# Performance work log

Measured on AMD Instinct MI355X. Metric: run time of the kernel, lower is better.

Reference implementation:

```python
import jax, jax.numpy as jnp
import numpy as np

B = 1024
P = 8
D = 2048
NUM_IDS = 64
MARGIN = 0.3
EPS = 1e-12


def setup_inputs() -> dict:
    key = jax.random.key(0)
    k1, k2, k3 = jax.random.split(key, 3)
    feats = jax.random.normal(k1, (B, P * D), dtype=jnp.float32)
    labels = jax.random.randint(k2, (B,), 0, NUM_IDS, dtype=jnp.int64)
    subs = jax.random.randint(k3, (B,), 0, 2, dtype=jnp.int64)
    return {"feats": feats, "labels": labels, "subs": subs}


def reference(feats, labels, subs):
    b = feats.shape[0]
    f = feats.reshape(b, -1, D)  # [B, P, D]
    dt = f.dtype

    # Per-sample class centers via a single segment-mean pass
    # (equivalent to the original per-sample boolean-mask mean loop).
    seg_sum = jax.ops.segment_sum(f, labels, num_segments=NUM_IDS)  # [NUM_IDS, P, D]
    counts = jax.ops.segment_sum(jnp.ones((b,), dt), labels, num_segments=NUM_IDS)
    centers_by_id = seg_sum / jnp.maximum(counts, 1.0)[:, None, None]
    centers = centers_by_id[labels]  # [B, P, D]

    # dist_ap[i] = sum_p ||f[i,p] - center[i,p]||
    d_ap = jnp.sqrt(jnp.clip(jnp.sum((f - centers) ** 2, axis=-1), EPS, None)).sum(-1)  # [B]
    dist_ap = d_ap[:, None] + d_ap[None, :]  # [B, B]

    # pairwise_distance: dist_aa[i,j] = sum_p ||f[i,p] - f[j,p]||, via gemm trick
    sq = jnp.sum(f * f, axis=-1)  # [B, P]
    inner = jnp.einsum('ipd,jpd->ijp', f, f)  # [B, B, P]
    d2 = sq[:, None, :] + sq[None, :, :] - 2.0 * inner
    dist_aa = jnp.sqrt(jnp.clip(d2, EPS, None)).sum(-1)  # [B, B]

    # masked margin loss over negative (different-label) pairs
    mask = labels[:, None] != labels[None, :]  # [B, B] bool
    vals = jnp.clip(dist_ap - dist_aa + MARGIN, 0.0, None)
    maskf = mask.astype(dt)
    loss = jnp.sum(vals * maskf) / jnp.sum(maskf)
    return loss
```

## Files before the change

### kernel.cpp

```cpp
#include <hip/hip_runtime.h>
#include <hip/hip_bf16.h>

#define B_ 1024
#define P_ 8
#define D_ 2048
#define FD_ (P_ * D_)
#define NID 64
#define MARGIN_ 0.3f
#define EPS_ 1e-12f

typedef unsigned short u16;
typedef float float4_t __attribute__((ext_vector_type(4)));

#define AS1 __attribute__((address_space(1)))
#define AS3 __attribute__((address_space(3)))

__device__ __forceinline__ float bf2f(u16 v) {
    unsigned x = (unsigned)v << 16;
    float f;
    __builtin_memcpy(&f, &x, 4);
    return f;
}

static const size_t OFF_COUNTS = 0;
static const size_t OFF_OFFS   = 256;
static const size_t OFF_PERM   = 512;
static const size_t OFF_NEG    = 4608;
static const size_t OFF_POS    = 8176;
static const size_t OFF_S      = 8192;
static const size_t OFF_SQ     = 40960;
static const size_t OFF_DAP    = 73728;
static const size_t OFF_FB     = 131072;
static const size_t OFF_PD     = OFF_FB + (size_t)B_ * FD_;

__global__ void k_counts(const int* __restrict__ labels, float* countsf, int* offs,
                         int* perm, float* negcnt) {
    __shared__ int h[NID], o[NID], cur[NID];
    int tid = threadIdx.x;
    if (tid < NID) h[tid] = 0;
    __syncthreads();
    for (int i = tid; i < B_; i += 256) atomicAdd(&h[labels[i]], 1);
    __syncthreads();
    if (tid == 0) {
        int acc = 0;
        long long ss = 0;
        for (int c = 0; c < NID; c++) {
            o[c] = acc;
            acc += h[c];
            ss += (long long)h[c] * h[c];
        }
        *negcnt = (float)((long long)B_ * B_ - ss);
    }
    __syncthreads();
    if (tid < NID) {
        countsf[tid] = (float)h[tid];
        offs[tid] = o[tid];
        cur[tid] = o[tid];
    }
    __syncthreads();
    for (int i = tid; i < B_; i += 256) {
        int pos = atomicAdd(&cur[labels[i]], 1);
        perm[pos] = i;
    }
}

__global__ void k_rowstats(const float* __restrict__ feats, unsigned char* __restrict__ fb,
                           float* __restrict__ sq) {
    int i = blockIdx.x;
    int tid = threadIdx.x;
    int w = tid >> 6, lane = tid & 63;
    const float* frow = feats + (size_t)i * FD_;
    unsigned char* brow = fb + (size_t)i * FD_;
#pragma unroll
    for (int pp = 0; pp < 2; pp++) {
        int p = w * 2 + pp;
        int off = p * D_;
        float s2 = 0.f;
#pragma unroll
        for (int ch = 0; ch < 8; ch++) {
            int d = off + ch * 256 + lane * 4;
            float4 f = *(const float4*)(frow + d);
            int pk = __builtin_amdgcn_cvt_pk_fp8_f32(f.x, f.y, 0, false);
            pk = __builtin_amdgcn_cvt_pk_fp8_f32(f.z, f.w, pk, true);
            *(unsigned int*)(brow + d) = (unsigned int)pk;
            s2 += f.x * f.x + f.y * f.y + f.z * f.z + f.w * f.w;
        }
        for (int o = 32; o; o >>= 1) s2 += __shfl_down(s2, o, 64);
        if (lane == 0) sq[i * P_ + p] = s2;
    }
}

__global__ __launch_bounds__(512, 4) void k_pairs(const unsigned char* __restrict__ fb,
                                                  const float* __restrict__ sq,
                                                  const int* __restrict__ labels,
                                                  float* __restrict__ S,
                                                  u16* __restrict__ pd) {
    const int i0 = blockIdx.y * 128, j0 = blockIdx.x * 128;
    const int p = blockIdx.z;
    __shared__ __align__(16) unsigned char smem[65536];
    __shared__ float sqAs[128], sqBs[128];
    __shared__ int labA[128], labB[128];
    const int tid = threadIdx.x;
    const int lane = tid & 63, wid = tid >> 6;
    const int s = wid & 3, h = wid >> 2;
    if (tid < 128) {
        sqAs[tid] = sq[(i0 + tid) * 8 + p];
        labA[tid] = labels[i0 + tid];
    } else if (tid < 256) {
        int t = tid - 128;
        sqBs[t] = sq[(j0 + t) * 8 + p];
        labB[t] = labels[j0 + t];
    }

    const int wi = (s >> 1) * 64, wj = (s & 1) * 64;
    const int lhi = lane >> 4, llo = lane & 15;
    const int sl = llo & 7;
    const int lr = lane >> 3;
    const int lc = (lane & 7) ^ lr;

    unsigned char* const As = smem + h * 16384;
    unsigned char* const Bs = smem + 32768 + h * 16384;

    const size_t colbase = (size_t)p * D_ + (size_t)h * 1024 + (size_t)lc * 16;
    const unsigned char* gA[4];
    const unsigned char* gB[4];
    unsigned char* lA[4];
    unsigned char* lB[4];
#pragma unroll
    for (int inst = 0; inst < 4; inst++) {
        int r0 = s * 32 + inst * 8;
        gA[inst] = fb + (size_t)(i0 + r0 + lr) * FD_ + colbase;
        gB[inst] = fb + (size_t)(j0 + r0 + lr) * FD_ + colbase;
        lA[inst] = As + r0 * 128;
        lB[inst] = Bs + r0 * 128;
    }

    float4_t acc[4][4];
#pragma unroll
    for (int a = 0; a < 4; a++)
#pragma unroll
        for (int b = 0; b < 4; b++) acc[a][b] = (float4_t){0.f, 0.f, 0.f, 0.f};

    for (int kb = 0; kb < 8; kb++) {
        const int koff = kb * 128;
        __syncthreads();
#pragma unroll
        for (int inst = 0; inst < 4; inst++) {
            __builtin_amdgcn_global_load_lds((const AS1 void*)(gA[inst] + koff),
                                             (AS3 void*)lA[inst], 16, 0, 0);
            __builtin_amdgcn_global_load_lds((const AS1 void*)(gB[inst] + koff),
                                             (AS3 void*)lB[inst], 16, 0, 0);
        }
        __syncthreads();
#pragma unroll
        for (int ks = 0; ks < 4; ks++) {
            const int pcb = ((2 * ks + (lhi >> 1)) ^ sl) * 16 + (lhi & 1) * 8;
            long af[4], bf[4];
#pragma unroll
            for (int a = 0; a < 4; a++) {
                af[a] = *(const long*)(As + (wi + a * 16 + llo) * 128 + pcb);
                bf[a] = *(const long*)(Bs + (wj + a * 16 + llo) * 128 + pcb);
            }
#pragma unroll
            for (int a = 0; a < 4; a++)
#pragma unroll
                for (int b = 0; b < 4; b++)
                    acc[a][b] = __builtin_amdgcn_mfma_f32_16x16x32_fp8_fp8(
                        af[a], bf[b], acc[a][b], 0, 0, 0);
        }
    }
    __syncthreads();
    float* ep = (float*)smem;
    if (h == 1) {
#pragma unroll
        for (int a = 0; a < 4; a++)
#pragma unroll
            for (int b = 0; b < 4; b++)
                *(float4_t*)&ep[(((s * 4 + a) * 4 + b) * 64 + lane) * 4] = acc[a][b];
    }
    __syncthreads();
    if (h == 0) {
        u16* outp = pd + (size_t)p * B_ * B_;
        float rs[4][4];
#pragma unroll
        for (int a = 0; a < 4; a++)
#pragma unroll
            for (int r = 0; r < 4; r++) rs[a][r] = 0.f;
#pragma unroll
        for (int a = 0; a < 4; a++) {
            int la0 = labA[wi + a * 16 + lhi * 4 + 0];
            int la1 = labA[wi + a * 16 + lhi * 4 + 1];
            int la2 = labA[wi + a * 16 + lhi * 4 + 2];
            int la3 = labA[wi + a * 16 + lhi * 4 + 3];
#pragma unroll
            for (int b = 0; b < 4; b++) {
                float4_t o = *(const float4_t*)&ep[(((s * 4 + a) * 4 + b) * 64 + lane) * 4];
                int lb = labB[wj + b * 16 + llo];
                int jl = wj + b * 16 + llo;
#pragma unroll
                for (int r = 0; r < 4; r++) {
                    int il = wi + a * 16 + lhi * 4 + r;
                    float t = acc[a][b][r] + o[r];
                    float d2 = sqAs[il] + sqBs[jl] - 2.0f * t;
                    outp[(size_t)(i0 + il) * B_ + (j0 + jl)] =
                        __bfloat16_as_ushort(__float2bfloat16(sqrtf(fmaxf(d2, EPS_))));
                    int la = (r == 0) ? la0 : (r == 1) ? la1 : (r == 2) ? la2 : la3;
                    if (lb == la) rs[a][r] += t;
                }
            }
        }
#pragma unroll
        for (int a = 0; a < 4; a++)
#pragma unroll
            for (int r = 0; r < 4; r++) {
                float v = rs[a][r];
                v += __shfl_xor(v, 1, 64);
                v += __shfl_xor(v, 2, 64);
                v += __shfl_xor(v, 4, 64);
                v += __shfl_xor(v, 8, 64);
                if (llo == 0)
                    atomicAdd(&S[(size_t)(i0 + wi + a * 16 + lhi * 4 + r) * 8 + p], v);
            }
    }
}

__global__ void k_dap(const float* __restrict__ S, const float* __restrict__ sq,
                      const float* __restrict__ countsf, const int* __restrict__ offs,
                      const int* __restrict__ perm, float* __restrict__ dap) {
    int c = blockIdx.x;
    int tid = threadIdx.x;
    int cnt = (int)countsf[c];
    int off = offs[c];
    __shared__ float T[8];
    if (tid < 8) {
        float t = 0.f;
        for (int m = 0; m < cnt; m++) t += S[(size_t)perm[off + m] * 8 + tid];
        T[tid] = t;
    }
    __syncthreads();
    float n = fmaxf((float)cnt, 1.f);
    float inv = 1.f / n, inv2 = inv * inv;
    for (int m = tid; m < cnt; m += 64) {
        int i = perm[off + m];
        float d = 0.f;
#pragma unroll
        for (int p = 0; p < 8; p++) {
            float d2 = sq[i * 8 + p] - 2.f * inv * S[(size_t)i * 8 + p] + inv2 * T[p];
            d += sqrtf(fmaxf(d2, EPS_));
        }
        dap[i] = d;
    }
}

__global__ void k_lossred(const u16* __restrict__ pd, const float* __restrict__ dap,
                          const int* __restrict__ labels, float* possum) {
    int i = blockIdx.x;
    int tid = threadIdx.x;
    float di = dap[i];
    int li = labels[i];
    float lsum = 0.f;
    for (int j = tid; j < B_; j += 256) {
        if (labels[j] != li) {
            float daa = 0.f;
#pragma unroll
            for (int p = 0; p < P_; p++)
                daa += bf2f(pd[(size_t)p * B_ * B_ + (size_t)i * B_ + j]);
            float v = di + dap[j] - daa + MARGIN_;
            lsum += fmaxf(v, 0.f);
        }
    }
    for (int o = 32; o; o >>= 1) lsum += __shfl_down(lsum, o, 64);
    __shared__ float red[4];
    int wid = tid >> 6, lane = tid & 63;
    if (lane == 0) red[wid] = lsum;
    __syncthreads();
    if (tid == 0) atomicAdd(possum, red[0] + red[1] + red[2] + red[3]);
}

__global__ void k_finalize(const float* possum, const float* negcnt, float* out) {
    out[0] = possum[0] / negcnt[0];
}

extern "C" void kernel_launch(void* const* d_in, const int* in_sizes, int n_in,
                              void* d_out, int out_size, void* d_ws, size_t ws_size,
                              hipStream_t stream) {
    const float* feats = (const float*)d_in[0];
    const int* labels  = (const int*)d_in[1];
    float* out = (float*)d_out;

    char* w = (char*)d_ws;
    float* countsf = (float*)(w + OFF_COUNTS);
    int* offs      = (int*)(w + OFF_OFFS);
    int* perm      = (int*)(w + OFF_PERM);
    float* negcnt  = (float*)(w + OFF_NEG);
    float* possum  = (float*)(w + OFF_POS);
    float* S       = (float*)(w + OFF_S);
    float* sq      = (float*)(w + OFF_SQ);
    float* dap     = (float*)(w + OFF_DAP);
    unsigned char* fb = (unsigned char*)(w + OFF_FB);
    u16* pd        = (u16*)(w + OFF_PD);

    hipMemsetAsync(w + OFF_POS, 0, (OFF_S - OFF_POS) + (size_t)B_ * P_ * 4, stream);

    k_counts<<<1, 256, 0, stream>>>(labels, countsf, offs, perm, negcnt);
    k_rowstats<<<B_, 256, 0, stream>>>(feats, fb, sq);
    k_pairs<<<dim3(8, 8, 8), 512, 0, stream>>>(fb, sq, labels, S, pd);
    k_dap<<<NID, 64, 0, stream>>>(S, sq, countsf, offs, perm, dap);
    k_lossred<<<B_, 256, 0, stream>>>(pd, dap, labels, possum);
    k_finalize<<<1, 1, 0, stream>>>(possum, negcnt, out);
}
```

Before: 169.5 us.

## Double-buffer FP8 GEMM LDS tiles, pre-permute fp8 layout, vectorize loss reduction

The fp8 conversion kernel now writes bytes in a permuted order so each lane can fetch 16-byte fragments that supply two MFMA k-steps. The pairwise GEMM uses smaller 64-byte k-slices in two LDS buffers, loading the next slice while computing the current one, with a new XOR swizzle. The loss reduction kernel reads four columns per thread using vector loads. This aims to hide global-to-LDS latency and cut LDS read instructions, but it adds index complexity and relies on the permuted layout matching the MFMA operand order exactly.

After: 173.7 us. 2.5% more time.

```diff
diff --git a/kernel.cpp b/kernel.cpp
--- a/kernel.cpp
+++ b/kernel.cpp
@@ -11,6 +11,7 @@
 
 typedef unsigned short u16;
 typedef float float4_t __attribute__((ext_vector_type(4)));
+typedef long long2_t __attribute__((ext_vector_type(2)));
 
 #define AS1 __attribute__((address_space(1)))
 #define AS3 __attribute__((address_space(3)))
@@ -71,6 +72,8 @@
     int w = tid >> 6, lane = tid & 63;
     const float* frow = feats + (size_t)i * FD_;
     unsigned char* brow = fb + (size_t)i * FD_;
+    const int wsel = (lane >> 4) * 64;
+    const int no = ((lane >> 1) & 3) * 16 + ((lane >> 3) & 1) * 8 + (lane & 1) * 4;
 #pragma unroll
     for (int pp = 0; pp < 2; pp++) {
         int p = w * 2 + pp;
@@ -82,7 +85,7 @@
             float4 f = *(const float4*)(frow + d);
             int pk = __builtin_amdgcn_cvt_pk_fp8_f32(f.x, f.y, 0, false);
             pk = __builtin_amdgcn_cvt_pk_fp8_f32(f.z, f.w, pk, true);
-            *(unsigned int*)(brow + d) = (unsigned int)pk;
+            *(unsigned int*)(brow + off + ch * 256 + wsel + no) = (unsigned int)pk;
             s2 += f.x * f.x + f.y * f.y + f.z * f.z + f.w * f.w;
         }
         for (int o = 32; o; o >>= 1) s2 += __shfl_down(s2, o, 64);
@@ -114,25 +117,29 @@
 
     const int wi = (s >> 1) * 64, wj = (s & 1) * 64;
     const int lhi = lane >> 4, llo = lane & 15;
-    const int sl = llo & 7;
-    const int lr = lane >> 3;
-    const int lc = (lane & 7) ^ lr;
-
-    unsigned char* const As = smem + h * 16384;
-    unsigned char* const Bs = smem + 32768 + h * 16384;
-
-    const size_t colbase = (size_t)p * D_ + (size_t)h * 1024 + (size_t)lc * 16;
-    const unsigned char* gA[4];
-    const unsigned char* gB[4];
-    unsigned char* lA[4];
-    unsigned char* lB[4];
-#pragma unroll
-    for (int inst = 0; inst < 4; inst++) {
-        int r0 = s * 32 + inst * 8;
-        gA[inst] = fb + (size_t)(i0 + r0 + lr) * FD_ + colbase;
-        gB[inst] = fb + (size_t)(j0 + r0 + lr) * FD_ + colbase;
-        lA[inst] = As + r0 * 128;
-        lB[inst] = Bs + r0 * 128;
+
+    const int srcsw = ((lane & 3) ^ ((lane >> 3) & 3)) << 4;
+    const size_t colbase = (size_t)p * D_ + (size_t)h * 1024 + srcsw;
+    const unsigned char* gA[2];
+    const unsigned char* gB[2];
+    unsigned char* lA[2];
+    unsigned char* lB[2];
+#pragma unroll
+    for (int inst = 0; inst < 2; inst++) {
+        const int r0 = s * 32 + inst * 16;
+        gA[inst] = fb + (size_t)(i0 + r0 + (lane >> 2)) * FD_ + colbase;
+        gB[inst] = fb + (size_t)(j0 + r0 + (lane >> 2)) * FD_ + colbase;
+        lA[inst] = smem + h * 8192 + r0 * 64;
+        lB[inst] = smem + 16384 + h * 8192 + r0 * 64;
+    }
+
+    const int csw = (lhi ^ ((llo >> 1) & 3)) << 4;
+    const unsigned char* aAddr[4];
+    const unsigned char* bAddr[4];
+#pragma unroll
+    for (int a = 0; a < 4; a++) {
+        aAddr[a] = smem + h * 8192 + (wi + a * 16 + llo) * 64 + csw;
+        bAddr[a] = smem + 16384 + h * 8192 + (wj + a * 16 + llo) * 64 + csw;
     }
 
     float4_t acc[4][4];
@@ -141,34 +148,54 @@
 #pragma unroll
         for (int b = 0; b < 4; b++) acc[a][b] = (float4_t){0.f, 0.f, 0.f, 0.f};
 
-    for (int kb = 0; kb < 8; kb++) {
-        const int koff = kb * 128;
+#define STAGE(BUF, KOFF)                                                                  \
+    {                                                                                     \
+        __builtin_amdgcn_global_load_lds((const AS1 void*)(gA[0] + (KOFF)),               \
+                                         (AS3 void*)(lA[0] + (BUF)*32768), 16, 0, 0);     \
+        __builtin_amdgcn_global_load_lds((const AS1 void*)(gB[0] + (KOFF)),               \
+                                         (AS3 void*)(lB[0] + (BUF)*32768), 16, 0, 0);     \
+        __builtin_amdgcn_global_load_lds((const AS1 void*)(gA[1] + (KOFF)),               \
+                                         (AS3 void*)(lA[1] + (BUF)*32768), 16, 0, 0);     \
+        __builtin_amdgcn_global_load_lds((const AS1 void*)(gB[1] + (KOFF)),               \
+                                         (AS3 void*)(lB[1] + (BUF)*32768), 16, 0, 0);     \
+    }
+
+#define COMPUTE(BUF)                                                                      \
+    {                                                                                     \
+        long2_t af[4], bq[4];                                                             \
+        _Pragma("unroll") for (int a = 0; a < 4; a++) {                                   \
+            af[a] = *(const long2_t*)(aAddr[a] + (BUF)*32768);                            \
+            bq[a] = *(const long2_t*)(bAddr[a] + (BUF)*32768);                            \
+        }                                                                                 \
+        _Pragma("unroll") for (int a = 0; a < 4; a++)                                     \
+            _Pragma("unroll") for (int b = 0; b < 4; b++)                                 \
+                acc[a][b] = __builtin_amdgcn_mfma_f32_16x16x32_fp8_fp8(                   \
+                    af[a].x, bq[b].x, acc[a][b], 0, 0, 0);                                \
+        _Pragma("unroll") for (int a = 0; a < 4; a++)                                     \
+            _Pragma("unroll") for (int b = 0; b < 4; b++)                                 \
+                acc[a][b] = __builtin_amdgcn_mfma_f32_16x16x32_fp8_fp8(                   \
+                    af[a].y, bq[b].y, acc[a][b], 0, 0, 0);                                \
+    }
+
+    STAGE(0, 0);
+    __syncthreads();
+#pragma unroll 1
+    for (int kb2 = 0; kb2 < 7; kb2++) {
+        STAGE(1, (kb2 * 2 + 1) * 64);
+        COMPUTE(0);
         __syncthreads();
-#pragma unroll
-        for (int inst = 0; inst < 4; inst++) {
-            __builtin_amdgcn_global_load_lds((const AS1 void*)(gA[inst] + koff),
-                                             (AS3 void*)lA[inst], 16, 0, 0);
-            __builtin_amdgcn_global_load_lds((const AS1 void*)(gB[inst] + koff),
-                                             (AS3 void*)lB[inst], 16, 0, 0);
-        }
+        STAGE(0, (kb2 * 2 + 2) * 64);
+        COMPUTE(1);
         __syncthreads();
-#pragma unroll
-        for (int ks = 0; ks < 4; ks++) {
-            const int pcb = ((2 * ks + (lhi >> 1)) ^ sl) * 16 + (lhi & 1) * 8;
-            long af[4], bf[4];
-#pragma unroll
-            for (int a = 0; a < 4; a++) {
-                af[a] = *(const long*)(As + (wi + a * 16 + llo) * 128 + pcb);
-                bf[a] = *(const long*)(Bs + (wj + a * 16 + llo) * 128 + pcb);
-            }
-#pragma unroll
-            for (int a = 0; a < 4; a++)
-#pragma unroll
-                for (int b = 0; b < 4; b++)
-                    acc[a][b] = __builtin_amdgcn_mfma_f32_16x16x32_fp8_fp8(
-                        af[a], bf[b], acc[a][b], 0, 0, 0);
-        }
-    }
+    }
+    STAGE(1, 15 * 64);
+    COMPUTE(0);
+    __syncthreads();
+    COMPUTE(1);
+
+#undef STAGE
+#undef COMPUTE
+
     __syncthreads();
     float* ep = (float*)smem;
     if (h == 1) {
@@ -258,17 +285,23 @@
     int tid = threadIdx.x;
     float di = dap[i];
     int li = labels[i];
+    int j0 = tid * 4;
+    float d0 = 0.f, d1 = 0.f, d2 = 0.f, d3 = 0.f;
+#pragma unroll
+    for (int p = 0; p < P_; p++) {
+        ushort4 v = *(const ushort4*)&pd[(size_t)p * B_ * B_ + (size_t)i * B_ + j0];
+        d0 += bf2f(v.x);
+        d1 += bf2f(v.y);
+        d2 += bf2f(v.z);
+        d3 += bf2f(v.w);
+    }
+    int4 lj = *(const int4*)&labels[j0];
+    float4 dj = *(const float4*)&dap[j0];
     float lsum = 0.f;
-    for (int j = tid; j < B_; j += 256) {
-        if (labels[j] != li) {
-            float daa = 0.f;
-#pragma unroll
-            for (int p = 0; p < P_; p++)
-                daa += bf2f(pd[(size_t)p * B_ * B_ + (size_t)i * B_ + j]);
-            float v = di + dap[j] - daa + MARGIN_;
-            lsum += fmaxf(v, 0.f);
-        }
-    }
+    if (lj.x != li) lsum += fmaxf(di + dj.x - d0 + MARGIN_, 0.f);
+    if (lj.y != li) lsum += fmaxf(di + dj.y - d1 + MARGIN_, 0.f);
+    if (lj.z != li) lsum += fmaxf(di + dj.z - d2 + MARGIN_, 0.f);
+    if (lj.w != li) lsum += fmaxf(di + dj.w - d3 + MARGIN_, 0.f);
     for (int o = 32; o; o >>= 1) lsum += __shfl_down(lsum, o, 64);
     __shared__ float red[4];
     int wid = tid >> 6, lane = tid & 63;
```

## Fuse launches: merge prep kernels, last-block dap tail, and fold finalize

Applied to the files above, without the earlier changes.

Merges the label-counting and row-stats kernels into one launch and drops the memset by zeroing accumulators inside the prep kernel. The dap computation moves into the last-finishing block of the pair kernel, found with an atomic done counter, and the final division moves into the last block of the loss reduction. The loss reduction also vectorises its pd, label and dap loads. This cuts the pipeline from six launches plus a memset to three, trading launch gaps for a serial tail in a single block and reliance on atomic counters for correctness.

New measurement: 183.3 us. 1.08x slower.

```diff
diff --git a/kernel.cpp b/kernel.cpp
--- a/kernel.cpp
+++ b/kernel.cpp
@@ -8,6 +8,7 @@
 #define NID 64
 #define MARGIN_ 0.3f
 #define EPS_ 1e-12f
+#define NPAIRBLK (8 * 8 * 8)
 
 typedef unsigned short u16;
 typedef float float4_t __attribute__((ext_vector_type(4)));
@@ -22,10 +23,13 @@
     return f;
 }
 
+__device__ __forceinline__ float coh_read(float* p) { return atomicAdd(p, 0.0f); }
+
 static const size_t OFF_COUNTS = 0;
 static const size_t OFF_OFFS   = 256;
 static const size_t OFF_PERM   = 512;
 static const size_t OFF_NEG    = 4608;
+static const size_t OFF_DONE   = 4616;
 static const size_t OFF_POS    = 8176;
 static const size_t OFF_S      = 8192;
 static const size_t OFF_SQ     = 40960;
@@ -33,10 +37,36 @@
 static const size_t OFF_FB     = 131072;
 static const size_t OFF_PD     = OFF_FB + (size_t)B_ * FD_;
 
-__global__ void k_counts(const int* __restrict__ labels, float* countsf, int* offs,
-                         int* perm, float* negcnt) {
+__global__ void k_prep(const float* __restrict__ feats, const int* __restrict__ labels,
+                       unsigned char* __restrict__ fb, float* __restrict__ sq,
+                       float* countsf, int* offs, int* perm, float* negcnt,
+                       float* S, float* possum, int* done) {
+    int tid = threadIdx.x;
+    if (blockIdx.x < B_) {
+        int i = blockIdx.x;
+        int w = tid >> 6, lane = tid & 63;
+        const float* frow = feats + (size_t)i * FD_;
+        unsigned char* brow = fb + (size_t)i * FD_;
+#pragma unroll
+        for (int pp = 0; pp < 2; pp++) {
+            int p = w * 2 + pp;
+            int off = p * D_;
+            float s2 = 0.f;
+#pragma unroll
+            for (int ch = 0; ch < 8; ch++) {
+                int d = off + ch * 256 + lane * 4;
+                float4 f = *(const float4*)(frow + d);
+                int pk = __builtin_amdgcn_cvt_pk_fp8_f32(f.x, f.y, 0, false);
+                pk = __builtin_amdgcn_cvt_pk_fp8_f32(f.z, f.w, pk, true);
+                *(unsigned int*)(brow + d) = (unsigned int)pk;
+                s2 += f.x * f.x + f.y * f.y + f.z * f.z + f.w * f.w;
+            }
+            for (int o = 32; o; o >>= 1) s2 += __shfl_down(s2, o, 64);
+            if (lane == 0) sq[i * P_ + p] = s2;
+        }
+        return;
+    }
     __shared__ int h[NID], o[NID], cur[NID];
-    int tid = threadIdx.x;
     if (tid < NID) h[tid] = 0;
     __syncthreads();
     for (int i = tid; i < B_; i += 256) atomicAdd(&h[labels[i]], 1);
@@ -50,6 +80,9 @@
             ss += (long long)h[c] * h[c];
         }
         *negcnt = (float)((long long)B_ * B_ - ss);
+        *possum = 0.f;
+        done[0] = 0;
+        done[1] = 0;
     }
     __syncthreads();
     if (tid < NID) {
@@ -62,39 +95,19 @@
         int pos = atomicAdd(&cur[labels[i]], 1);
         perm[pos] = i;
     }
-}
-
-__global__ void k_rowstats(const float* __restrict__ feats, unsigned char* __restrict__ fb,
-                           float* __restrict__ sq) {
-    int i = blockIdx.x;
-    int tid = threadIdx.x;
-    int w = tid >> 6, lane = tid & 63;
-    const float* frow = feats + (size_t)i * FD_;
-    unsigned char* brow = fb + (size_t)i * FD_;
-#pragma unroll
-    for (int pp = 0; pp < 2; pp++) {
-        int p = w * 2 + pp;
-        int off = p * D_;
-        float s2 = 0.f;
-#pragma unroll
-        for (int ch = 0; ch < 8; ch++) {
-            int d = off + ch * 256 + lane * 4;
-            float4 f = *(const float4*)(frow + d);
-            int pk = __builtin_amdgcn_cvt_pk_fp8_f32(f.x, f.y, 0, false);
-            pk = __builtin_amdgcn_cvt_pk_fp8_f32(f.z, f.w, pk, true);
-            *(unsigned int*)(brow + d) = (unsigned int)pk;
-            s2 += f.x * f.x + f.y * f.y + f.z * f.z + f.w * f.w;
-        }
-        for (int o = 32; o; o >>= 1) s2 += __shfl_down(s2, o, 64);
-        if (lane == 0) sq[i * P_ + p] = s2;
-    }
+    for (int i = tid; i < B_ * P_; i += 256) S[i] = 0.f;
 }
 
 __global__ __launch_bounds__(512, 4) void k_pairs(const unsigned char* __restrict__ fb,
                                                   const float* __restrict__ sq,
                                                   const int* __restrict__ labels,
                                                   float* __restrict__ S,
-                                                  u16* __restrict__ pd) {
+                                                  u16* __restrict__ pd,
+                                                  const float* __restrict__ countsf,
+                                                  const int* __restrict__ offs,
+                                                  const int* __restrict__ perm,
+                                                  float* __restrict__ dap,
+                                                  int* __restrict__ done) {
     const int i0 = blockIdx.y * 128, j0 = blockIdx.x * 128;
     const int p = blockIdx.z;
     __shared__ __align__(16) unsigned char smem[65536];
@@ -222,63 +235,86 @@
                     atomicAdd(&S[(size_t)(i0 + wi + a * 16 + lhi * 4 + r) * 8 + p], v);
             }
     }
-}
-
-__global__ void k_dap(const float* __restrict__ S, const float* __restrict__ sq,
-                      const float* __restrict__ countsf, const int* __restrict__ offs,
-                      const int* __restrict__ perm, float* __restrict__ dap) {
-    int c = blockIdx.x;
-    int tid = threadIdx.x;
-    int cnt = (int)countsf[c];
-    int off = offs[c];
-    __shared__ float T[8];
-    if (tid < 8) {
+
+    __syncthreads();
+    int* lastFlag = (int*)smem;
+    float* Tl = (float*)(smem + 64);
+    float* cntl = (float*)(smem + 64 + 2048);
+    if (tid == 0) {
+        __threadfence();
+        int v = atomicAdd(done, 1);
+        lastFlag[0] = (v == NPAIRBLK - 1) ? 1 : 0;
+    }
+    __syncthreads();
+    if (!lastFlag[0]) return;
+    {
+        int c = tid >> 3, pp = tid & 7;
+        int cnt = (int)countsf[c];
+        int off = offs[c];
         float t = 0.f;
-        for (int m = 0; m < cnt; m++) t += S[(size_t)perm[off + m] * 8 + tid];
-        T[tid] = t;
-    }
-    __syncthreads();
-    float n = fmaxf((float)cnt, 1.f);
-    float inv = 1.f / n, inv2 = inv * inv;
-    for (int m = tid; m < cnt; m += 64) {
-        int i = perm[off + m];
-        float d = 0.f;
-#pragma unroll
-        for (int p = 0; p < 8; p++) {
-            float d2 = sq[i * 8 + p] - 2.f * inv * S[(size_t)i * 8 + p] + inv2 * T[p];
-            d += sqrtf(fmaxf(d2, EPS_));
-        }
-        dap[i] = d;
+#pragma unroll 4
+        for (int m = 0; m < cnt; m++) {
+            int idx = perm[off + m];
+            t += coh_read(&S[(size_t)idx * 8 + pp]);
+        }
+        Tl[c * 8 + pp] = t;
+        if (pp == 0) cntl[c] = fmaxf((float)cnt, 1.f);
+    }
+    __syncthreads();
+    for (int i = tid; i < B_; i += 512) {
+        int c = labels[i];
+        float n = cntl[c];
+        float inv = 1.f / n, inv2 = inv * inv;
+        float dsum = 0.f;
+#pragma unroll
+        for (int pp = 0; pp < 8; pp++) {
+            float Sv = coh_read(&S[(size_t)i * 8 + pp]);
+            float d2 = sq[i * 8 + pp] - 2.f * inv * Sv + inv2 * Tl[c * 8 + pp];
+            dsum += sqrtf(fmaxf(d2, EPS_));
+        }
+        dap[i] = dsum;
     }
 }
 
 __global__ void k_lossred(const u16* __restrict__ pd, const float* __restrict__ dap,
-                          const int* __restrict__ labels, float* possum) {
+                          const int* __restrict__ labels, float* possum,
+                          const float* __restrict__ negcnt, int* __restrict__ done,
+                          float* __restrict__ out) {
     int i = blockIdx.x;
     int tid = threadIdx.x;
     float di = dap[i];
     int li = labels[i];
+    int j0 = tid * 4;
+    float d0 = 0.f, d1 = 0.f, d2 = 0.f, d3 = 0.f;
+#pragma unroll
+    for (int p = 0; p < P_; p++) {
+        ushort4 v = *(const ushort4*)&pd[(size_t)p * B_ * B_ + (size_t)i * B_ + j0];
+        d0 += bf2f(v.x);
+        d1 += bf2f(v.y);
+        d2 += bf2f(v.z);
+        d3 += bf2f(v.w);
+    }
+    int4 lj = *(const int4*)&labels[j0];
+    float4 dj = *(const float4*)&dap[j0];
     float lsum = 0.f;
-    for (int j = tid; j < B_; j += 256) {
-        if (labels[j] != li) {
-            float daa = 0.f;
-#pragma unroll
-            for (int p = 0; p < P_; p++)
-                daa += bf2f(pd[(size_t)p * B_ * B_ + (size_t)i * B_ + j]);
-            float v = di + dap[j] - daa + MARGIN_;
-            lsum += fmaxf(v, 0.f);
-        }
-    }
+    if (lj.x != li) lsum += fmaxf(di + dj.x - d0 + MARGIN_, 0.f);
+    if (lj.y != li) lsum += fmaxf(di + dj.y - d1 + MARGIN_, 0.f);
+    if (lj.z != li) lsum += fmaxf(di + dj.z - d2 + MARGIN_, 0.f);
+    if (lj.w != li) lsum += fmaxf(di + dj.w - d3 + MARGIN_, 0.f);
     for (int o = 32; o; o >>= 1) lsum += __shfl_down(lsum, o, 64);
     __shared__ float red[4];
     int wid = tid >> 6, lane = tid & 63;
     if (lane == 0) red[wid] = lsum;
     __syncthreads();
-    if (tid == 0) atomicAdd(possum, red[0] + red[1] + red[2] + red[3]);
-}
-
-__global__ void k_finalize(const float* possum, const float* negcnt, float* out) {
-    out[0] = possum[0] / negcnt[0];
+    if (tid == 0) {
+        atomicAdd(possum, red[0] + red[1] + red[2] + red[3]);
+        __threadfence();
+        int v = atomicAdd(done, 1);
+        if (v == B_ - 1) {
+            float ps = atomicAdd(possum, 0.f);
+            out[0] = ps / negcnt[0];
+        }
+    }
 }
 
 extern "C" void kernel_launch(void* const* d_in, const int* in_sizes, int n_in,
@@ -293,6 +329,7 @@
     int* offs      = (int*)(w + OFF_OFFS);
     int* perm      = (int*)(w + OFF_PERM);
     float* negcnt  = (float*)(w + OFF_NEG);
+    int* done      = (int*)(w + OFF_DONE);
     float* possum  = (float*)(w + OFF_POS);
     float* S       = (float*)(w + OFF_S);
     float* sq      = (float*)(w + OFF_SQ);
@@ -300,12 +337,9 @@
     unsigned char* fb = (unsigned char*)(w + OFF_FB);
     u16* pd        = (u16*)(w + OFF_PD);
 
-    hipMemsetAsync(w + OFF_POS, 0, (OFF_S - OFF_POS) + (size_t)B_ * P_ * 4, stream);
-
-    k_counts<<<1, 256, 0, stream>>>(labels, countsf, offs, perm, negcnt);
-    k_rowstats<<<B_, 256, 0, stream>>>(feats, fb, sq);
-    k_pairs<<<dim3(8, 8, 8), 512, 0, stream>>>(fb, sq, labels, S, pd);
-    k_dap<<<NID, 64, 0, stream>>>(S, sq, countsf, offs, perm, dap);
-    k_lossred<<<B_, 256, 0, stream>>>(pd, dap, labels, possum);
-    k_finalize<<<1, 1, 0, stream>>>(possum, negcnt, out);
-}
+    k_prep<<<B_ + 1, 256, 0, stream>>>(feats, labels, fb, sq, countsf, offs, perm,
+                                       negcnt, S, possum, done);
+    k_pairs<<<dim3(8, 8, 8), 512, 0, stream>>>(fb, sq, labels, S, pd, countsf, offs,
+                                               perm, dap, done);
+    k_lossred<<<B_, 256, 0, stream>>>(pd, dap, labels, possum, negcnt, done + 1, out);
+}
```
